# Kernel tuning notes

Hardware: AMD Instinct MI355X
Metric: run time of the kernel (lower is better)

The kernel has to match this reference:

```python
import jax, jax.numpy as jnp
import numpy as np

BATCH, SEQ, DMODEL, DSTATE = 4, 2048, 1024, 16


def _hippo_legs(N):
    # HiPPO-LegS: A[n,k] = -sqrt(2n+1)sqrt(2k+1) for n>k, -(n+1) on diag; B[n]=sqrt(2n+1)
    n = np.arange(N)
    b = np.sqrt(2.0 * n + 1.0)
    A = -np.tril(np.outer(b, b), -1) - np.diag(n + 1.0)
    return A.astype(np.float32), b.astype(np.float32)


def setup_inputs() -> dict:
    key = jax.random.key(0)
    x = jax.random.normal(key, (BATCH, SEQ, DMODEL), dtype=jnp.float32)
    A_c, B_c = _hippo_legs(DSTATE)
    dt = 1.0 / float(SEQ)  # simple Euler discretization of the continuous HiPPO ODE
    A = jnp.eye(DSTATE, dtype=jnp.float32) + dt * jnp.asarray(A_c)
    Bvec = dt * jnp.asarray(B_c)
    return {"x": x, "A": A, "Bvec": Bvec}


def reference(x, A, Bvec):
    # x: (B, L, D); A: (N, N) discrete transition; Bvec: (N,) input map.
    # Selective-scan recurrence per channel: h_t = A h_{t-1} + Bvec * x_t, y_t = <Bvec, h_t>
    B, L, D = x.shape
    N = Bvec.shape[0]

    def step(h, xt):
        # h: (B, D, N), xt: (B, D)
        h = jnp.einsum('mn,bdn->bdm', A, h) + xt[..., None] * Bvec
        y = h @ Bvec  # (B, D)
        return h, y

    h0 = jnp.zeros((B, D, N), dtype=x.dtype)
    _, ys = jax.lax.scan(step, h0, jnp.moveaxis(x, 1, 0))  # ys: (L, B, D)
    return jnp.moveaxis(ys, 0, 1)  # (B, L, D)
```

## Files before the change

kernel.cpp:

```cpp
#include <hip/hip_runtime.h>

#define BATCH  4
#define SEQL   2048
#define DMODEL 1024
#define NST    16
#define CT     64
#define NCH    (SEQL / CT)

#define WS_P     0
#define WS_W     1024
#define WS_KV    2048
#define WS_APOW  2176
#define WS_HIN   4096
#define WS_CBUF  (WS_HIN + BATCH * NCH * DMODEL * 16)

__global__ __launch_bounds__(256) void setup_tables(const float* __restrict__ A,
                                                    const float* __restrict__ Bv,
                                                    float* __restrict__ ws) {
    __shared__ double buf0[256], buf1[256], buf2[256], buf3[256];
    __shared__ double bd[16], vtmp[16];
    double* S  = buf0;
    double* R  = buf1;
    double* Ta = buf2;
    double* Tb = buf3;
    const int t  = threadIdx.x;
    const int i  = t >> 4;
    const int kk = t & 15;
    const int delta = blockIdx.x;

    S[t] = (double)A[t];
    R[t] = (i == kk) ? 1.0 : 0.0;
    if (t < 16) bd[t] = (double)Bv[t];
    __syncthreads();

    for (int sb = 0; sb < 7; ++sb) {
        if ((delta >> sb) & 1) {
            double acc = 0.0;
            #pragma unroll
            for (int l = 0; l < 16; ++l) acc += R[i * 16 + l] * S[l * 16 + kk];
            Ta[t] = acc;
            __syncthreads();
            double* tmp = R; R = Ta; Ta = tmp;
        }
        if (sb < 6) {
            double acc = 0.0;
            #pragma unroll
            for (int l = 0; l < 16; ++l) acc += S[i * 16 + l] * S[l * 16 + kk];
            Tb[t] = acc;
            __syncthreads();
            double* tmp = S; S = Tb; Tb = tmp;
        }
    }

    if (delta < CT) {
        if (t < 16) {
            double acc = 0.0;
            #pragma unroll
            for (int k = 0; k < 16; ++k) acc += R[t * 16 + k] * bd[k];
            ws[WS_P + (CT - 1 - delta) * 16 + t] = (float)acc;
            vtmp[t] = acc;
        }
        __syncthreads();
        if (t == 0) {
            double kd = 0.0;
            for (int m = 0; m < 16; ++m) kd += bd[m] * vtmp[m];
            ws[WS_KV + 63 + delta] = (float)kd;
        }
    }
    if (delta >= 1 && t < 16) {
        double acc = 0.0;
        #pragma unroll
        for (int n = 0; n < 16; ++n) acc += bd[n] * R[n * 16 + t];
        ws[WS_W + (delta - 1) * 16 + t] = (float)acc;
    }
    if (delta == CT) ws[WS_APOW + t] = (float)R[t];
    if (delta == 0 && t < 63) ws[WS_KV + t] = 0.0f;
}

__global__ __launch_bounds__(256) void k1_chunkstate(const float* __restrict__ x,
                                                     float* __restrict__ ws) {
    const int blk  = blockIdx.x;
    const int b    = blk >> 7;
    const int j    = (blk >> 2) & 31;
    const int dblk = blk & 3;
    const int d    = dblk * 256 + threadIdx.x;

    const float* P  = ws + WS_P;
    const float* xp = x + ((size_t)(b * SEQL + j * CT)) * DMODEL + d;

    float c[16];
    #pragma unroll
    for (int m = 0; m < 16; ++m) c[m] = 0.0f;

    float xa[8], xb[8];
    #pragma unroll
    for (int s = 0; s < 8; ++s) xa[s] = xp[(size_t)s * DMODEL];

    #pragma unroll
    for (int g = 0; g < 8; ++g) {
        float* cur = (g & 1) ? xb : xa;
        float* nxt = (g & 1) ? xa : xb;
        if (g < 7) {
            #pragma unroll
            for (int s = 0; s < 8; ++s)
                nxt[s] = xp[(size_t)((g + 1) * 8 + s) * DMODEL];
        }
        #pragma unroll
        for (int s = 0; s < 8; ++s) {
            const int ss = g * 8 + s;
            #pragma unroll
            for (int m = 0; m < 16; ++m)
                c[m] = fmaf(P[ss * 16 + m], cur[s], c[m]);
        }
    }

    float4* outp = (float4*)(ws + WS_CBUF + (((size_t)(b * NCH + j) * DMODEL) + d) * 16);
    #pragma unroll
    for (int q = 0; q < 4; ++q)
        outp[q] = make_float4(c[4 * q], c[4 * q + 1], c[4 * q + 2], c[4 * q + 3]);
}

__global__ __launch_bounds__(256) void k2_carry(float* __restrict__ ws) {
    const int blk = blockIdx.x;
    const int b   = blk >> 6;
    const int d0  = (blk & 63) * 16;
    const int t   = threadIdx.x;
    const int m   = t & 15;
    const int ch  = t >> 4;
    const int d   = d0 + ch;
    const int laneBase = t & 48;

    const float* cbuf   = ws + WS_CBUF;
    const size_t base0   = (((size_t)(b * NCH) * DMODEL) + d) * 16 + m;
    const size_t jstride = (size_t)DMODEL * 16;

    float cpre[NCH];
    #pragma unroll
    for (int j = 0; j < NCH; ++j)
        cpre[j] = cbuf[base0 + (size_t)j * jstride];

    float Arow[16];
    #pragma unroll
    for (int k = 0; k < 16; ++k) Arow[k] = ws[WS_APOW + m * 16 + k];

    float* hin = ws + WS_HIN;
    float s = 0.0f;
    #pragma unroll
    for (int j = 0; j < NCH; ++j) {
        hin[base0 + (size_t)j * jstride] = s;
        float acc = cpre[j];
        #pragma unroll
        for (int k = 0; k < 16; ++k)
            acc = fmaf(Arow[k], __shfl(s, laneBase + k, 64), acc);
        s = acc;
    }
}

template <int TT>
__device__ __forceinline__ void k3_body(const float* __restrict__ xs,
                                        const float* __restrict__ ws,
                                        float* __restrict__ y,
                                        int b, int j, int d, int dl) {
    const float* hinp = ws + WS_HIN + (((size_t)(b * NCH + j) * DMODEL) + d) * 16;
    float4 hv[4];
    #pragma unroll
    for (int q = 0; q < 4; ++q) hv[q] = ((const float4*)hinp)[q];

    float h[16];
    #pragma unroll
    for (int q = 0; q < 4; ++q) {
        h[4 * q]     = hv[q].x; h[4 * q + 1] = hv[q].y;
        h[4 * q + 2] = hv[q].z; h[4 * q + 3] = hv[q].w;
    }

    const float* W = ws + WS_W + TT * 16 * 16;
    float yv[16];
    #pragma unroll
    for (int i = 0; i < 16; ++i) {
        float acc = 0.0f;
        #pragma unroll
        for (int m = 0; m < 16; ++m) acc = fmaf(W[i * 16 + m], h[m], acc);
        yv[i] = acc;
    }

    __syncthreads();

    const float* kv63 = ws + WS_KV + 63;
    #pragma unroll
    for (int ss = 0; ss < (TT + 1) * 16; ++ss) {
        const float xv = xs[ss * 64 + dl];
        #pragma unroll
        for (int i = 0; i < 16; ++i) {
            if (TT * 16 + i >= ss)
                yv[i] = fmaf(kv63[TT * 16 + i - ss], xv, yv[i]);
        }
    }

    float* yp = y + ((size_t)(b * SEQL + j * CT + TT * 16)) * DMODEL + d;
    #pragma unroll
    for (int i = 0; i < 16; ++i) yp[(size_t)i * DMODEL] = yv[i];
}

__global__ __launch_bounds__(256, 8) void k3_output(const float* __restrict__ x,
                                                    const float* __restrict__ ws,
                                                    float* __restrict__ y) {
    __shared__ __align__(16) float xs[CT * 64];
    const int blk  = blockIdx.x;
    const int b    = blk >> 9;
    const int j    = (blk >> 4) & 31;
    const int dblk = blk & 15;
    const int t    = threadIdx.x;
    const int tq   = t >> 6;
    const int dl   = t & 63;
    const int d    = dblk * 64 + dl;

    {
        const float* xp = x + ((size_t)(b * SEQL + j * CT)) * DMODEL + dblk * 64;
        #pragma unroll
        for (int k = 0; k < 4; ++k) {
            const int f     = k * 256 + t;
            const int sigma = f >> 4;
            const int c4    = f & 15;
            *(float4*)(&xs[sigma * 64 + c4 * 4]) =
                *(const float4*)(xp + (size_t)sigma * DMODEL + c4 * 4);
        }
    }

    switch (tq) {
        case 0: k3_body<0>(xs, ws, y, b, j, d, dl); break;
        case 1: k3_body<1>(xs, ws, y, b, j, d, dl); break;
        case 2: k3_body<2>(xs, ws, y, b, j, d, dl); break;
        default: k3_body<3>(xs, ws, y, b, j, d, dl); break;
    }
}

extern "C" void kernel_launch(void* const* d_in, const int* in_sizes, int n_in,
                              void* d_out, int out_size, void* d_ws, size_t ws_size,
                              hipStream_t stream) {
    (void)in_sizes; (void)n_in; (void)out_size; (void)ws_size;
    const float* x  = (const float*)d_in[0];
    const float* A  = (const float*)d_in[1];
    const float* Bv = (const float*)d_in[2];
    float* out = (float*)d_out;
    float* ws  = (float*)d_ws;

    setup_tables<<<65, 256, 0, stream>>>(A, Bv, ws);
    k1_chunkstate<<<512, 256, 0, stream>>>(x, ws);
    k2_carry<<<256, 256, 0, stream>>>(ws);
    k3_output<<<2048, 256, 0, stream>>>(x, ws, out);
}
```

Baseline: 123.2 us.

## Fuse table setup, chunk-state and carry scan into one kernel

Merges the three preceding kernels (table precomputation, per-chunk state reduction, inter-chunk carry scan) into a single kernel. Each block recomputes the power tables redundantly in shared memory, then streams x chunk by chunk, computing the chunk state on the fly and feeding it straight into the carry recurrence. This removes two launches and the write and re-read of the chunk-state buffer. The cost is redundant table work in every block and a serial loop over chunks with only 256 blocks, so there is less parallelism for reading x.

```diff
diff --git a/kernel.cpp b/kernel.cpp
--- a/kernel.cpp
+++ b/kernel.cpp
@@ -7,148 +7,127 @@
 #define CT     64
 #define NCH    (SEQL / CT)
 
-#define WS_P     0
 #define WS_W     1024
 #define WS_KV    2048
-#define WS_APOW  2176
 #define WS_HIN   4096
-#define WS_CBUF  (WS_HIN + BATCH * NCH * DMODEL * 16)
-
-__global__ __launch_bounds__(256) void setup_tables(const float* __restrict__ A,
-                                                    const float* __restrict__ Bv,
-                                                    float* __restrict__ ws) {
-    __shared__ double buf0[256], buf1[256], buf2[256], buf3[256];
-    __shared__ double bd[16], vtmp[16];
-    double* S  = buf0;
-    double* R  = buf1;
-    double* Ta = buf2;
-    double* Tb = buf3;
-    const int t  = threadIdx.x;
-    const int i  = t >> 4;
-    const int kk = t & 15;
-    const int delta = blockIdx.x;
-
-    S[t] = (double)A[t];
-    R[t] = (i == kk) ? 1.0 : 0.0;
-    if (t < 16) bd[t] = (double)Bv[t];
+
+__global__ __launch_bounds__(256) void ka_tables_scan(const float* __restrict__ x,
+                                                      const float* __restrict__ Ain,
+                                                      const float* __restrict__ Bvin,
+                                                      float* __restrict__ ws) {
+    __shared__ double M[256], Mt[256];
+    __shared__ double Vd[64][16];
+    __shared__ double Wd[65][16];
+    __shared__ double bd[16];
+    __shared__ float  Pl[64][16];
+    __shared__ float  Ap[256];
+    __shared__ __align__(16) float xs[16][68];
+
+    const int t   = threadIdx.x;
+    const int blk = blockIdx.x;
+    const int b   = blk >> 6;
+    const int g   = blk & 63;
+    const int d0  = g * 16;
+
+    M[t] = (double)Ain[t];
+    if (t < 16) {
+        bd[t]    = (double)Bvin[t];
+        Vd[0][t] = (double)Bvin[t];
+        Wd[0][t] = (double)Bvin[t];
+    }
     __syncthreads();
 
-    for (int sb = 0; sb < 7; ++sb) {
-        if ((delta >> sb) & 1) {
+    #pragma unroll
+    for (int k = 0; k < 6; ++k) {
+        const int cnt = 1 << k;
+        const int m   = t & 15;
+        for (int dd = t >> 4; dd < cnt; dd += 16) {
+            double av = 0.0, aw = 0.0;
+            #pragma unroll
+            for (int l = 0; l < 16; ++l) {
+                av += M[m * 16 + l] * Vd[dd][l];
+                aw += Wd[dd][l] * M[l * 16 + m];
+            }
+            Vd[dd + cnt][m] = av;
+            Wd[dd + cnt][m] = aw;
+        }
+        __syncthreads();
+        {
+            const int i = t >> 4, jj = t & 15;
             double acc = 0.0;
             #pragma unroll
-            for (int l = 0; l < 16; ++l) acc += R[i * 16 + l] * S[l * 16 + kk];
-            Ta[t] = acc;
-            __syncthreads();
-            double* tmp = R; R = Ta; Ta = tmp;
-        }
-        if (sb < 6) {
-            double acc = 0.0;
-            #pragma unroll
-            for (int l = 0; l < 16; ++l) acc += S[i * 16 + l] * S[l * 16 + kk];
-            Tb[t] = acc;
-            __syncthreads();
-            double* tmp = S; S = Tb; Tb = tmp;
-        }
-    }
-
-    if (delta < CT) {
-        if (t < 16) {
-            double acc = 0.0;
-            #pragma unroll
-            for (int k = 0; k < 16; ++k) acc += R[t * 16 + k] * bd[k];
-            ws[WS_P + (CT - 1 - delta) * 16 + t] = (float)acc;
-            vtmp[t] = acc;
-        }
-        __syncthreads();
-        if (t == 0) {
-            double kd = 0.0;
-            for (int m = 0; m < 16; ++m) kd += bd[m] * vtmp[m];
-            ws[WS_KV + 63 + delta] = (float)kd;
-        }
-    }
-    if (delta >= 1 && t < 16) {
-        double acc = 0.0;
-        #pragma unroll
-        for (int n = 0; n < 16; ++n) acc += bd[n] * R[n * 16 + t];
-        ws[WS_W + (delta - 1) * 16 + t] = (float)acc;
-    }
-    if (delta == CT) ws[WS_APOW + t] = (float)R[t];
-    if (delta == 0 && t < 63) ws[WS_KV + t] = 0.0f;
-}
-
-__global__ __launch_bounds__(256) void k1_chunkstate(const float* __restrict__ x,
-                                                     float* __restrict__ ws) {
-    const int blk  = blockIdx.x;
-    const int b    = blk >> 7;
-    const int j    = (blk >> 2) & 31;
-    const int dblk = blk & 3;
-    const int d    = dblk * 256 + threadIdx.x;
-
-    const float* P  = ws + WS_P;
-    const float* xp = x + ((size_t)(b * SEQL + j * CT)) * DMODEL + d;
-
-    float c[16];
-    #pragma unroll
-    for (int m = 0; m < 16; ++m) c[m] = 0.0f;
-
-    float xa[8], xb[8];
-    #pragma unroll
-    for (int s = 0; s < 8; ++s) xa[s] = xp[(size_t)s * DMODEL];
-
-    #pragma unroll
-    for (int g = 0; g < 8; ++g) {
-        float* cur = (g & 1) ? xb : xa;
-        float* nxt = (g & 1) ? xa : xb;
-        if (g < 7) {
-            #pragma unroll
-            for (int s = 0; s < 8; ++s)
-                nxt[s] = xp[(size_t)((g + 1) * 8 + s) * DMODEL];
-        }
-        #pragma unroll
-        for (int s = 0; s < 8; ++s) {
-            const int ss = g * 8 + s;
-            #pragma unroll
-            for (int m = 0; m < 16; ++m)
-                c[m] = fmaf(P[ss * 16 + m], cur[s], c[m]);
-        }
-    }
-
-    float4* outp = (float4*)(ws + WS_CBUF + (((size_t)(b * NCH + j) * DMODEL) + d) * 16);
-    #pragma unroll
-    for (int q = 0; q < 4; ++q)
-        outp[q] = make_float4(c[4 * q], c[4 * q + 1], c[4 * q + 2], c[4 * q + 3]);
-}
-
-__global__ __launch_bounds__(256) void k2_carry(float* __restrict__ ws) {
-    const int blk = blockIdx.x;
-    const int b   = blk >> 6;
-    const int d0  = (blk & 63) * 16;
-    const int t   = threadIdx.x;
-    const int m   = t & 15;
-    const int ch  = t >> 4;
-    const int d   = d0 + ch;
+            for (int l = 0; l < 16; ++l) acc += M[i * 16 + l] * M[l * 16 + jj];
+            Mt[t] = acc;
+            if (k == 5 && t < 16) {
+                double aw = 0.0;
+                #pragma unroll
+                for (int l = 0; l < 16; ++l) aw += Wd[32][l] * M[l * 16 + t];
+                Wd[64][t] = aw;
+            }
+        }
+        __syncthreads();
+        M[t] = Mt[t];
+        __syncthreads();
+    }
+
+    Ap[t] = (float)M[t];
+    for (int e = t; e < 1024; e += 256) {
+        const int r = e >> 4, mm = e & 15;
+        Pl[r][mm] = (float)Vd[63 - r][mm];
+        ws[WS_W + e] = (float)Wd[r + 1][mm];
+    }
+    if (t < 64) {
+        double kd = 0.0;
+        #pragma unroll
+        for (int mm = 0; mm < 16; ++mm) kd += bd[mm] * Vd[t][mm];
+        ws[WS_KV + 63 + t] = (float)kd;
+    }
+    __syncthreads();
+
+    const int ch = t >> 4;
+    const int m  = t & 15;
+    const int d  = d0 + ch;
     const int laneBase = t & 48;
-
-    const float* cbuf   = ws + WS_CBUF;
-    const size_t base0   = (((size_t)(b * NCH) * DMODEL) + d) * 16 + m;
-    const size_t jstride = (size_t)DMODEL * 16;
-
-    float cpre[NCH];
-    #pragma unroll
-    for (int j = 0; j < NCH; ++j)
-        cpre[j] = cbuf[base0 + (size_t)j * jstride];
+    const int sigt = t >> 2;
+    const int c4   = t & 3;
+
+    float Preg[64];
+    #pragma unroll
+    for (int sg = 0; sg < 64; ++sg) Preg[sg] = Pl[sg][m];
 
     float Arow[16];
     #pragma unroll
-    for (int k = 0; k < 16; ++k) Arow[k] = ws[WS_APOW + m * 16 + k];
-
+    for (int k = 0; k < 16; ++k) Arow[k] = Ap[m * 16 + k];
+
+    const float* xb = x + (size_t)(b * SEQL) * DMODEL + d0;
     float* hin = ws + WS_HIN;
+
+    float4 cur = *(const float4*)(xb + (size_t)sigt * DMODEL + c4 * 4);
+
     float s = 0.0f;
-    #pragma unroll
     for (int j = 0; j < NCH; ++j) {
-        hin[base0 + (size_t)j * jstride] = s;
-        float acc = cpre[j];
+        __syncthreads();
+        xs[c4 * 4 + 0][sigt] = cur.x;
+        xs[c4 * 4 + 1][sigt] = cur.y;
+        xs[c4 * 4 + 2][sigt] = cur.z;
+        xs[c4 * 4 + 3][sigt] = cur.w;
+        __syncthreads();
+        if (j + 1 < NCH)
+            cur = *(const float4*)(xb + (size_t)((j + 1) * CT + sigt) * DMODEL + c4 * 4);
+
+        float c = 0.0f;
+        #pragma unroll
+        for (int sg = 0; sg < 16; ++sg) {
+            const float4 xv = *(const float4*)(&xs[ch][sg * 4]);
+            c = fmaf(Preg[4 * sg + 0], xv.x, c);
+            c = fmaf(Preg[4 * sg + 1], xv.y, c);
+            c = fmaf(Preg[4 * sg + 2], xv.z, c);
+            c = fmaf(Preg[4 * sg + 3], xv.w, c);
+        }
+
+        hin[(((size_t)(b * NCH + j) * DMODEL) + d0) * 16 + t] = s;
+
+        float acc = c;
         #pragma unroll
         for (int k = 0; k < 16; ++k)
             acc = fmaf(Arow[k], __shfl(s, laneBase + k, 64), acc);
@@ -220,9 +199,9 @@
         for (int k = 0; k < 4; ++k) {
             const int f     = k * 256 + t;
             const int sigma = f >> 4;
-            const int c4    = f & 15;
-            *(float4*)(&xs[sigma * 64 + c4 * 4]) =
-                *(const float4*)(xp + (size_t)sigma * DMODEL + c4 * 4);
+            const int cc    = f & 15;
+            *(float4*)(&xs[sigma * 64 + cc * 4]) =
+                *(const float4*)(xp + (size_t)sigma * DMODEL + cc * 4);
         }
     }
 
@@ -244,8 +223,6 @@
     float* out = (float*)d_out;
     float* ws  = (float*)d_ws;
 
-    setup_tables<<<65, 256, 0, stream>>>(A, Bv, ws);
-    k1_chunkstate<<<512, 256, 0, stream>>>(x, ws);
-    k2_carry<<<256, 256, 0, stream>>>(ws);
+    ka_tables_scan<<<256, 256, 0, stream>>>(x, A, Bv, ws);
     k3_output<<<2048, 256, 0, stream>>>(x, ws, out);
 }
```

Measured after the change: 119.1 us. 3.3% less time.
